# Kernel tuning notes

Measured on AMD Instinct MI355X. Metric: run time of the kernel, lower is better.

Reference implementation:

```python
import jax, jax.numpy as jnp
import numpy as np

EPS = 1e-6
TEMP_GEO = 0.07
W_LOCAL = 0.5
W_SHARP = 0.5


def _l2norm(x):
    return x / jnp.clip(jnp.linalg.norm(x, axis=-1, keepdims=True), 1e-12)


def setup_inputs() -> dict:
    key = jax.random.key(0)
    ks = jax.random.split(key, 6)
    B, L, S, C = 8, 1024, 1024, 128
    N, P = 8, 256
    q_geo = _l2norm(jax.random.normal(ks[0], (B, L, C), jnp.float32))
    geo_pos = _l2norm(jax.random.normal(ks[1], (B, S, C), jnp.float32))
    label = jax.random.randint(ks[2], (B, L, S), 0, 2, jnp.int32)
    q_cl = jax.random.normal(ks[3], (N, P, C), jnp.float32)
    cl_pos = jax.random.normal(ks[4], (N, P, C), jnp.float32)
    idx = jax.random.randint(ks[5], (N,), 0, P, jnp.int32)
    return {"q_geo": q_geo, "q_cl": q_cl, "geo_pos": geo_pos,
            "cl_pos": cl_pos, "label": label, "idx": idx}


def _masked_mean(v, m):
    # per-sample mean over the [L,S] plane of entries where m is True
    m = m.astype(v.dtype)
    return jnp.sum(v * m, axis=(1, 2)) / jnp.maximum(jnp.sum(m, axis=(1, 2)), 1.0)


def _loftr_loss(conf, label):
    # standard LoFTR coarse CE loss (LoFTRLoss source absent from repo snippet)
    conf = jnp.clip(conf, EPS, 1.0 - EPS)
    pos = label == 1
    neg = label == 0
    pos_loss = _masked_mean(-jnp.log(conf), pos)          # [B]
    neg_loss = _masked_mean(-jnp.log(1.0 - conf), neg)    # [B]
    loss = pos_loss + neg_loss
    return jnp.mean(loss), jnp.mean(pos_loss), jnp.mean(neg_loss)


def _geometric_loss(q, k, label):
    sim = jnp.einsum('blc,bsc->bls', q, k) / TEMP_GEO        # [B,L,S]
    conf = jax.nn.softmax(sim, axis=1) * jax.nn.softmax(sim, axis=2)
    return _loftr_loss(conf, label)


def _sharpness_loss(q, k, label):
    sim = (1.0 + jnp.einsum('blc,bsc->bls', q, k)) / 2.0     # [B,L,S]
    # column stats (over L, dim=0 per sample) -> sharpness1 [B,S]
    s1 = (jnp.max(sim, axis=1) - jnp.mean(sim, axis=1)) / jnp.std(sim, axis=1, ddof=1)
    sharp1 = jax.nn.softmax(s1, axis=-1)
    # row stats (over S, dim=1 per sample) -> sharpness2 [B,L]
    s2 = (jnp.max(sim, axis=2) - jnp.mean(sim, axis=2)) / jnp.std(sim, axis=2, ddof=1)
    sharp2 = jax.nn.softmax(s2, axis=-1)
    simc = jnp.clip(sim, EPS, 1.0 - EPS)
    nll = -jnp.log(simc)
    pos = (label == 1).astype(simc.dtype)
    neg = (label == 0)
    loss1 = jnp.sum(nll * sharp1[:, None, :] * pos, axis=(1, 2))   # [B]
    loss2 = jnp.sum(nll * sharp2[:, :, None] * pos, axis=(1, 2))   # [B]
    loss3 = _masked_mean(-jnp.log(1.0 - simc), neg)                # [B]
    losses = (loss1 + loss2) / 2.0 + loss3
    return sharp1, jnp.mean(losses)


def _contrast_loss(q, all_k):
    # intended math of GeCoContrast: full cosine matrix, diag positives, tail negatives
    N = q.shape[0]
    sim = (1.0 + _l2norm(q) @ _l2norm(all_k).T) / 2.0   # [N, M]
    sim = jnp.clip(sim, EPS, 1.0 - EPS)
    l_pos = jnp.diagonal(sim[:, :N])                    # [N]
    l_neg = sim[:, N:]                                  # [N, M-N]
    return (jnp.mean(-jnp.log(l_pos)) + jnp.mean(-jnp.log(1.0 - l_neg))) / 2.0


def _forward(q_geo, q_cl, geo_pos, cl_pos, label, idx):
    loss_geo, geo_pos_loss, geo_neg_loss = _geometric_loss(q_geo, geo_pos, label)
    sharpness, loss_sharp = _sharpness_loss(q_geo, geo_pos, label)
    loss_geo = ((1.0 - W_SHARP) * loss_geo + W_SHARP * loss_sharp) * W_LOCAL

    N, P, C = q_cl.shape
    ar = jnp.arange(N)
    q_sel = q_cl[ar, idx]                               # [N,C]
    sel = cl_pos[ar, idx]                               # [N,C] positives moved to slot 0
    first = cl_pos[:, 0, :]
    swapped = cl_pos.at[ar, idx].set(first).at[:, 0, :].set(sel)
    cl_pos_save = sel
    all_k = jnp.concatenate([swapped[:, 0, :],
                             swapped[:, 1:, :].reshape(N * (P - 1), C)], axis=0)
    loss_cl = _contrast_loss(q_sel, all_k) * (1.0 - W_LOCAL)

    total = loss_geo + loss_cl
    return (sharpness, cl_pos_save, total, geo_pos_loss, geo_neg_loss, loss_sharp, loss_cl)


def reference(q_geo, q_cl, geo_pos, cl_pos, label, idx):
    return _forward(q_geo, q_cl, geo_pos, cl_pos, label, idx)
```

## Files before the change

### kernel.cpp

```cpp
#include <hip/hip_runtime.h>
#include <math.h>

#define BB 8
#define LL 1024
#define SS 1024
#define CC 128
#define NN 8
#define PP 256

static constexpr float EPS       = 1e-6f;
static constexpr float ONE_M_EPS = 1.0f - 1e-6f;
static constexpr float INV_T     = 1.0f / 0.07f;
static constexpr float NLL_MAX   = 13.815511f;
static constexpr float NLL_MIN   = 1.0000005e-6f;

static constexpr size_t DOTSZ      = (size_t)BB * LL * SS;
static constexpr size_t OFF_LSER   = DOTSZ;
static constexpr size_t OFF_S2RAW  = DOTSZ + 8192;
static constexpr size_t OFF_LSEC   = DOTSZ + 16384;
static constexpr size_t OFF_S1RAW  = DOTSZ + 24576;
static constexpr size_t OFF_SHARP2 = DOTSZ + 32768;
static constexpr size_t OFF_RP     = DOTSZ + 40960;
static constexpr size_t OFF_CP     = OFF_RP + 524288;
static constexpr size_t OFF_ACC    = OFF_CP + 524288;
static constexpr size_t OFF_ACCCL  = OFF_ACC + 48;
static constexpr size_t OFF_QN     = OFF_ACC + 64;

static constexpr int OUT_CLSAVE = 8192;
static constexpr int OUT_SCAL   = 9216;

typedef __bf16 bf16x8 __attribute__((ext_vector_type(8)));
typedef float  floatx4 __attribute__((ext_vector_type(4)));

__device__ __forceinline__ bf16x8 mkfrag(unsigned a, unsigned b, unsigned c, unsigned d) {
    uint4 t = make_uint4(a, b, c, d);
    return __builtin_bit_cast(bf16x8, t);
}

__device__ __forceinline__ void split_f4(float4 x,
                                         unsigned& hp0, unsigned& hp1,
                                         unsigned& lp0, unsigned& lp1) {
    unsigned u0 = __builtin_bit_cast(unsigned, x.x);
    unsigned u1 = __builtin_bit_cast(unsigned, x.y);
    unsigned u2 = __builtin_bit_cast(unsigned, x.z);
    unsigned u3 = __builtin_bit_cast(unsigned, x.w);
    unsigned r0 = u0 + 0x7FFFu + ((u0 >> 16) & 1u);
    unsigned r1 = u1 + 0x7FFFu + ((u1 >> 16) & 1u);
    unsigned r2 = u2 + 0x7FFFu + ((u2 >> 16) & 1u);
    unsigned r3 = u3 + 0x7FFFu + ((u3 >> 16) & 1u);
    float s0 = x.x - __builtin_bit_cast(float, r0 & 0xFFFF0000u);
    float s1 = x.y - __builtin_bit_cast(float, r1 & 0xFFFF0000u);
    float s2 = x.z - __builtin_bit_cast(float, r2 & 0xFFFF0000u);
    float s3 = x.w - __builtin_bit_cast(float, r3 & 0xFFFF0000u);
    hp0 = __builtin_amdgcn_perm(r1, r0, 0x07060302u);
    hp1 = __builtin_amdgcn_perm(r3, r2, 0x07060302u);
    lp0 = __builtin_amdgcn_perm(__builtin_bit_cast(unsigned, s1),
                                __builtin_bit_cast(unsigned, s0), 0x07060302u);
    lp1 = __builtin_amdgcn_perm(__builtin_bit_cast(unsigned, s3),
                                __builtin_bit_cast(unsigned, s2), 0x07060302u);
}

__global__ __launch_bounds__(512) void prep(const float* __restrict__ q_cl,
                                            const float* __restrict__ cl_pos,
                                            const int* __restrict__ idx,
                                            float* __restrict__ out, float* __restrict__ ws) {
    int tid = threadIdx.x;
    if (tid < 50) ws[OFF_ACC + tid] = 0.0f;
    int n = tid >> 6, lane = tid & 63;
    int in = idx[n];
    const float* q = q_cl + ((size_t)(n * PP + in)) * CC;
    float2 qv = *(const float2*)(q + 2 * lane);
    float ss = qv.x * qv.x + qv.y * qv.y;
    for (int o = 32; o; o >>= 1) ss += __shfl_xor(ss, o);
    float inv = 1.0f / fmaxf(sqrtf(ss), 1e-12f);
    *(float2*)(ws + OFF_QN + n * 128 + 2 * lane) = make_float2(qv.x * inv, qv.y * inv);
    const float* cp = cl_pos + ((size_t)(n * PP + in)) * CC;
    float2 cv = *(const float2*)(cp + 2 * lane);
    *(float2*)(out + OUT_CLSAVE + n * 128 + 2 * lane) = cv;
}

__global__ __launch_bounds__(256) void gemm_dot(const float* __restrict__ A,
                                                const float* __restrict__ Bm,
                                                float* __restrict__ dot,
                                                float* __restrict__ ws) {
    int tid  = threadIdx.x;
    int lane = tid & 63;
    int w    = tid >> 6;
    int t    = blockIdx.x * 4 + w;
    int b    = t >> 8;
    int rem  = t & 255;
    int lt   = rem >> 4, st = rem & 15;
    int l0   = lt * 64, s0 = st * 64;
    int fl   = lane & 15;
    int quad = lane >> 4;

    const float* Ab = A  + ((size_t)b * LL + l0) * CC;
    const float* Bb = Bm + ((size_t)b * SS + s0) * CC;

    floatx4 acc[4][4];
#pragma unroll
    for (int i = 0; i < 4; i++)
#pragma unroll
        for (int j = 0; j < 4; j++) acc[i][j] = (floatx4){0.f, 0.f, 0.f, 0.f};

    for (int c0 = 0; c0 < 128; c0 += 32) {
        float4 ax[4][2], bx[4][2];
#pragma unroll
        for (int mt = 0; mt < 4; mt++) {
            const float* p = Ab + (size_t)(mt * 16 + fl) * CC + c0 + quad * 8;
            ax[mt][0] = *(const float4*)p;
            ax[mt][1] = *(const float4*)(p + 4);
        }
#pragma unroll
        for (int nt = 0; nt < 4; nt++) {
            const float* p = Bb + (size_t)(nt * 16 + fl) * CC + c0 + quad * 8;
            bx[nt][0] = *(const float4*)p;
            bx[nt][1] = *(const float4*)(p + 4);
        }
        bf16x8 ah[4], al[4];
#pragma unroll
        for (int mt = 0; mt < 4; mt++) {
            unsigned h0, h1, h2, h3, q0, q1, q2, q3;
            split_f4(ax[mt][0], h0, h1, q0, q1);
            split_f4(ax[mt][1], h2, h3, q2, q3);
            ah[mt] = mkfrag(h0, h1, h2, h3);
            al[mt] = mkfrag(q0, q1, q2, q3);
        }
#pragma unroll
        for (int nt = 0; nt < 4; nt++) {
            unsigned h0, h1, h2, h3, q0, q1, q2, q3;
            split_f4(bx[nt][0], h0, h1, q0, q1);
            split_f4(bx[nt][1], h2, h3, q2, q3);
            bf16x8 bh = mkfrag(h0, h1, h2, h3);
            bf16x8 bl = mkfrag(q0, q1, q2, q3);
#pragma unroll
            for (int mt = 0; mt < 4; mt++) {
                acc[mt][nt] = __builtin_amdgcn_mfma_f32_16x16x32_bf16(ah[mt], bh, acc[mt][nt], 0, 0, 0);
                acc[mt][nt] = __builtin_amdgcn_mfma_f32_16x16x32_bf16(ah[mt], bl, acc[mt][nt], 0, 0, 0);
                acc[mt][nt] = __builtin_amdgcn_mfma_f32_16x16x32_bf16(al[mt], bh, acc[mt][nt], 0, 0, 0);
            }
        }
    }

    float* D = dot + ((size_t)b * LL + l0) * SS + s0;
#pragma unroll
    for (int mt = 0; mt < 4; mt++)
#pragma unroll
        for (int nt = 0; nt < 4; nt++) {
            int col = nt * 16 + fl;
#pragma unroll
            for (int r = 0; r < 4; r++) {
                int row = mt * 16 + quad * 4 + r;
                D[(size_t)row * SS + col] = acc[mt][nt][r];
            }
        }

    float ces[4], cmx[4], csm[4], csq[4];
#pragma unroll
    for (int nt = 0; nt < 4; nt++) { ces[nt] = 0.f; cmx[nt] = -1e30f; csm[nt] = 0.f; csq[nt] = 0.f; }
#pragma unroll
    for (int mt = 0; mt < 4; mt++) {
#pragma unroll
        for (int r = 0; r < 4; r++) {
            float es = 0.f, mx = -1e30f, sm = 0.f, sq = 0.f;
#pragma unroll
            for (int nt = 0; nt < 4; nt++) {
                float d  = acc[mt][nt][r];
                float e  = __expf(d * INV_T);
                float s2 = fmaf(0.5f, d, 0.5f);
                es += e; mx = fmaxf(mx, s2); sm += s2; sq += s2 * s2;
                ces[nt] += e; cmx[nt] = fmaxf(cmx[nt], s2); csm[nt] += s2; csq[nt] += s2 * s2;
            }
            for (int o = 1; o < 16; o <<= 1) {
                es += __shfl_xor(es, o);
                mx = fmaxf(mx, __shfl_xor(mx, o));
                sm += __shfl_xor(sm, o);
                sq += __shfl_xor(sq, o);
            }
            if (fl == 0) {
                int row = l0 + mt * 16 + quad * 4 + r;
                *(float4*)(ws + OFF_RP + (((size_t)(b * 16 + st)) * 1024 + row) * 4) =
                    make_float4(es, mx, sm, sq);
            }
        }
    }
#pragma unroll
    for (int nt = 0; nt < 4; nt++) {
        float es = ces[nt], mx = cmx[nt], sm = csm[nt], sq = csq[nt];
        for (int o = 16; o < 64; o <<= 1) {
            es += __shfl_xor(es, o);
            mx = fmaxf(mx, __shfl_xor(mx, o));
            sm += __shfl_xor(sm, o);
            sq += __shfl_xor(sq, o);
        }
        if (quad == 0) {
            int col = s0 + nt * 16 + fl;
            *(float4*)(ws + OFF_CP + (((size_t)(b * 16 + lt)) * 1024 + col) * 4) =
                make_float4(es, mx, sm, sq);
        }
    }
}

__global__ __launch_bounds__(256) void rc_combine(float* __restrict__ ws) {
    int g = (blockIdx.x & 31) * 256 + threadIdx.x;
    bool docol = blockIdx.x >= 32;
    int b = g >> 10, i = g & 1023;
    const float* part = ws + (docol ? OFF_CP : OFF_RP);
    float es = 0.f, mx = -1e30f, sm = 0.f, sq = 0.f;
#pragma unroll
    for (int t = 0; t < 16; t++) {
        float4 v = *(const float4*)(part + (((size_t)(b * 16 + t)) * 1024 + i) * 4);
        es += v.x; mx = fmaxf(mx, v.y); sm += v.z; sq += v.w;
    }
    float mean = sm * (1.0f / 1024.0f);
    float var  = (sq - sm * sm * (1.0f / 1024.0f)) * (1.0f / 1023.0f);
    float zs   = (mx - mean) / sqrtf(fmaxf(var, 1e-30f));
    if (!docol) {
        ws[OFF_LSER + g]  = __logf(es);
        ws[OFF_S2RAW + g] = zs;
    } else {
        ws[OFF_LSEC + g]  = __logf(es);
        ws[OFF_S1RAW + g] = zs;
    }
}

__global__ __launch_bounds__(256) void softmax16(float* __restrict__ ws, float* __restrict__ out) {
    int q = blockIdx.x;
    int b = q & 7;
    const float* src = ws + ((q < 8) ? OFF_S1RAW : OFF_S2RAW) + (size_t)b * 1024;
    float* dst = (q < 8) ? (out + (size_t)b * 1024) : (ws + OFF_SHARP2 + (size_t)b * 1024);
    float4 v = ((const float4*)src)[threadIdx.x];
    int lane = threadIdx.x & 63, wid = threadIdx.x >> 6;
    __shared__ float sb[4];
    __shared__ float red;
    float mx = fmaxf(fmaxf(v.x, v.y), fmaxf(v.z, v.w));
    for (int o = 32; o; o >>= 1) mx = fmaxf(mx, __shfl_xor(mx, o));
    if (!lane) sb[wid] = mx;
    __syncthreads();
    if (threadIdx.x == 0) red = fmaxf(fmaxf(sb[0], sb[1]), fmaxf(sb[2], sb[3]));
    __syncthreads();
    mx = red;
    float e0 = __expf(v.x - mx), e1 = __expf(v.y - mx), e2 = __expf(v.z - mx), e3 = __expf(v.w - mx);
    float sm = e0 + e1 + e2 + e3;
    for (int o = 32; o; o >>= 1) sm += __shfl_xor(sm, o);
    __syncthreads();
    if (!lane) sb[wid] = sm;
    __syncthreads();
    if (threadIdx.x == 0) red = sb[0] + sb[1] + sb[2] + sb[3];
    __syncthreads();
    float inv = 1.0f / red;
    ((float4*)dst)[threadIdx.x] = make_float4(e0 * inv, e1 * inv, e2 * inv, e3 * inv);
}

__device__ __forceinline__ void proc_elem(float d, int lab, float lcj, float sh1j,
                                          float lr, float s2v,
                                          float& posg, float& negg, float& l1, float& l2,
                                          float& negs, float& pcf) {
    float t = lr + lcj - d * (2.0f * INV_T);
    float isPos = (lab == 1) ? 1.0f : 0.0f;
    float isNeg = 1.0f - isPos;
    float tp   = fminf(fmaxf(t, NLL_MIN), NLL_MAX);
    float simc = fminf(fmaxf(fmaf(0.5f, d, 0.5f), EPS), ONE_M_EPS);
    float om   = fminf(fmaxf(fmaf(-0.5f, d, 0.5f), EPS), ONE_M_EPS);
    float nll2 = -__logf(simc);
    float cf   = fminf(fmaxf(__expf(-t), EPS), ONE_M_EPS);
    float nllg = -__logf(1.0f - cf);
    float nlls = -__logf(om);
    posg += isPos * tp;
    l1   += isPos * nll2 * sh1j;
    l2   += isPos * nll2 * s2v;
    pcf  += isPos;
    negg += isNeg * nllg;
    negs += isNeg * nlls;
}

__global__ __launch_bounds__(256) void main_loss(const float* __restrict__ dot,
                                                 const int* __restrict__ label,
                                                 const float* __restrict__ sharp1,
                                                 float* __restrict__ ws) {
    int b = blockIdx.y;
    int l0 = blockIdx.x * 4;
    int s = threadIdx.x * 4;
    float4 lc4 = *(const float4*)(ws + OFF_LSEC + (size_t)b * 1024 + s);
    float4 sh1 = *(const float4*)(sharp1 + (size_t)b * 1024 + s);
    const float* lser = ws + OFF_LSER + (size_t)b * 1024;
    const float* sh2  = ws + OFF_SHARP2 + (size_t)b * 1024;
    float posg = 0, negg = 0, l1 = 0, l2 = 0, negs = 0, pcf = 0;
#pragma unroll
    for (int r = 0; r < 4; r++) {
        int l = l0 + r;
        float lr  = lser[l];
        float s2v = sh2[l];
        size_t base = ((size_t)(b * 1024 + l)) * 1024 + s;
        float4 d4 = *(const float4*)(dot + base);
        int4  lb  = *(const int4*)(label + base);
        proc_elem(d4.x, lb.x, lc4.x, sh1.x, lr, s2v, posg, negg, l1, l2, negs, pcf);
        proc_elem(d4.y, lb.y, lc4.y, sh1.y, lr, s2v, posg, negg, l1, l2, negs, pcf);
        proc_elem(d4.z, lb.z, lc4.z, sh1.z, lr, s2v, posg, negg, l1, l2, negs, pcf);
        proc_elem(d4.w, lb.w, lc4.w, sh1.w, lr, s2v, posg, negg, l1, l2, negs, pcf);
    }
    float vals[6] = {posg, negg, l1, l2, negs, pcf};
    __shared__ float sb[6][4];
    int lane = threadIdx.x & 63, wid = threadIdx.x >> 6;
#pragma unroll
    for (int k = 0; k < 6; k++) {
        float v = vals[k];
        for (int o = 32; o; o >>= 1) v += __shfl_xor(v, o);
        if (!lane) sb[k][wid] = v;
    }
    __syncthreads();
    if (threadIdx.x < 6) {
        float r = sb[threadIdx.x][0] + sb[threadIdx.x][1] + sb[threadIdx.x][2] + sb[threadIdx.x][3];
        atomicAdd(ws + OFF_ACC + (size_t)b * 6 + threadIdx.x, r);
    }
}

__global__ __launch_bounds__(256) void contrast(const float* __restrict__ cl_pos,
                                                const int* __restrict__ idx,
                                                float* __restrict__ ws) {
    int j = blockIdx.x * 4 + (threadIdx.x >> 6);
    int lane = threadIdx.x & 63;
    int m, p;
    if (j < NN) {
        m = j; p = idx[j];
    } else {
        int jj = j - NN;
        m = jj / (PP - 1);
        p = 1 + (jj - m * (PP - 1));
        if (p == idx[m]) p = 0;
    }
    const float* k = cl_pos + ((size_t)(m * PP + p)) * CC;
    float2 kv = *(const float2*)(k + 2 * lane);
    float ksq = kv.x * kv.x + kv.y * kv.y;
    for (int o = 32; o; o >>= 1) ksq += __shfl_xor(ksq, o);
    float invkn = 1.0f / fmaxf(sqrtf(ksq), 1e-12f);
    float pos = 0.0f, neg = 0.0f;
    if (j < NN) {
        const float2 qv = *(const float2*)(ws + OFF_QN + j * 128 + 2 * lane);
        float dt = qv.x * kv.x + qv.y * kv.y;
        for (int o = 32; o; o >>= 1) dt += __shfl_xor(dt, o);
        float sim = fminf(fmaxf(fmaf(0.5f * invkn, dt, 0.5f), EPS), ONE_M_EPS);
        pos = -__logf(sim);
    } else {
#pragma unroll
        for (int n = 0; n < NN; n++) {
            const float2 qv = *(const float2*)(ws + OFF_QN + n * 128 + 2 * lane);
            float dt = qv.x * kv.x + qv.y * kv.y;
            for (int o = 32; o; o >>= 1) dt += __shfl_xor(dt, o);
            float om = fminf(fmaxf(fmaf(-0.5f * invkn, dt, 0.5f), EPS), ONE_M_EPS);
            neg -= __logf(om);
        }
    }
    __shared__ float sb[2][4];
    int w = threadIdx.x >> 6;
    if (!lane) { sb[0][w] = pos; sb[1][w] = neg; }
    __syncthreads();
    if (threadIdx.x == 0) {
        float ps = sb[0][0] + sb[0][1] + sb[0][2] + sb[0][3];
        float ng = sb[1][0] + sb[1][1] + sb[1][2] + sb[1][3];
        if (ps != 0.0f) atomicAdd(ws + OFF_ACCCL + 0, ps);
        if (ng != 0.0f) atomicAdd(ws + OFF_ACCCL + 1, ng);
    }
}

__global__ void finalize(float* __restrict__ out, const float* __restrict__ ws) {
    if (threadIdx.x != 0) return;
    float gp = 0, gn = 0, lsh = 0;
    for (int b = 0; b < 8; b++) {
        const float* a = ws + OFF_ACC + (size_t)b * 6;
        float pc = a[5];
        float nc = (float)((size_t)LL * SS) - pc;
        gp += a[0] / fmaxf(pc, 1.0f);
        gn += a[1] / fmaxf(nc, 1.0f);
        lsh += (a[2] + a[3]) * 0.5f + a[4] / fmaxf(nc, 1.0f);
    }
    gp *= 0.125f; gn *= 0.125f; lsh *= 0.125f;
    float lgeo = gp + gn;
    float lgw = (0.5f * lgeo + 0.5f * lsh) * 0.5f;
    float clp = ws[OFF_ACCCL + 0] / 8.0f;
    float cln = ws[OFF_ACCCL + 1] / (8.0f * 2040.0f);
    float lcl = (clp + cln) * 0.5f * 0.5f;
    out[OUT_SCAL + 0] = lgw + lcl;
    out[OUT_SCAL + 1] = gp;
    out[OUT_SCAL + 2] = gn;
    out[OUT_SCAL + 3] = lsh;
    out[OUT_SCAL + 4] = lcl;
}

extern "C" void kernel_launch(void* const* d_in, const int* in_sizes, int n_in,
                              void* d_out, int out_size, void* d_ws, size_t ws_size,
                              hipStream_t stream) {
    const float* q_geo   = (const float*)d_in[0];
    const float* q_cl    = (const float*)d_in[1];
    const float* geo_pos = (const float*)d_in[2];
    const float* cl_pos  = (const float*)d_in[3];
    const int*   label   = (const int*)d_in[4];
    const int*   idx     = (const int*)d_in[5];
    float* out = (float*)d_out;
    float* ws  = (float*)d_ws;
    float* dot = ws;

    prep<<<dim3(1), dim3(512), 0, stream>>>(q_cl, cl_pos, idx, out, ws);
    gemm_dot<<<dim3(512), dim3(256), 0, stream>>>(q_geo, geo_pos, dot, ws);
    rc_combine<<<dim3(64), dim3(256), 0, stream>>>(ws);
    softmax16<<<dim3(16), dim3(256), 0, stream>>>(ws, out);
    main_loss<<<dim3(256, 8), dim3(256), 0, stream>>>(dot, label, out, ws);
    contrast<<<dim3(512), dim3(256), 0, stream>>>(cl_pos, idx, ws);
    finalize<<<dim3(1), dim3(64), 0, stream>>>(out, ws);
}
```

Baseline: 163.7 us.

## Merge seven kernel launches into three with fused contrast, combine and finalize

Folds the prep and contrastive-loss work into extra blocks of the GEMM kernel, so they run alongside the GEMM tiles. Merges the row/column partial combine with the sharpness softmax into one kernel. Finalizes the scalar losses from the last main-loss block through an atomic completion counter instead of a separate launch. This removes launch overhead and serialization of small kernels, at the cost of a counter reset in the first kernel and extra synchronization logic.

```diff
diff --git a/kernel.cpp b/kernel.cpp
--- a/kernel.cpp
+++ b/kernel.cpp
@@ -16,15 +16,13 @@
 
 static constexpr size_t DOTSZ      = (size_t)BB * LL * SS;
 static constexpr size_t OFF_LSER   = DOTSZ;
-static constexpr size_t OFF_S2RAW  = DOTSZ + 8192;
 static constexpr size_t OFF_LSEC   = DOTSZ + 16384;
-static constexpr size_t OFF_S1RAW  = DOTSZ + 24576;
 static constexpr size_t OFF_SHARP2 = DOTSZ + 32768;
 static constexpr size_t OFF_RP     = DOTSZ + 40960;
 static constexpr size_t OFF_CP     = OFF_RP + 524288;
 static constexpr size_t OFF_ACC    = OFF_CP + 524288;
-static constexpr size_t OFF_ACCCL  = OFF_ACC + 48;
-static constexpr size_t OFF_QN     = OFF_ACC + 64;
+static constexpr size_t OFF_DONE   = OFF_ACC + 48;
+static constexpr size_t OFF_CLP    = OFF_ACC + 64;
 
 static constexpr int OUT_CLSAVE = 8192;
 static constexpr int OUT_SCAL   = 9216;
@@ -60,196 +58,241 @@
                                 __builtin_bit_cast(unsigned, s2), 0x07060302u);
 }
 
-__global__ __launch_bounds__(512) void prep(const float* __restrict__ q_cl,
-                                            const float* __restrict__ cl_pos,
-                                            const int* __restrict__ idx,
-                                            float* __restrict__ out, float* __restrict__ ws) {
-    int tid = threadIdx.x;
-    if (tid < 50) ws[OFF_ACC + tid] = 0.0f;
-    int n = tid >> 6, lane = tid & 63;
-    int in = idx[n];
-    const float* q = q_cl + ((size_t)(n * PP + in)) * CC;
-    float2 qv = *(const float2*)(q + 2 * lane);
-    float ss = qv.x * qv.x + qv.y * qv.y;
-    for (int o = 32; o; o >>= 1) ss += __shfl_xor(ss, o);
-    float inv = 1.0f / fmaxf(sqrtf(ss), 1e-12f);
-    *(float2*)(ws + OFF_QN + n * 128 + 2 * lane) = make_float2(qv.x * inv, qv.y * inv);
-    const float* cp = cl_pos + ((size_t)(n * PP + in)) * CC;
-    float2 cv = *(const float2*)(cp + 2 * lane);
-    *(float2*)(out + OUT_CLSAVE + n * 128 + 2 * lane) = cv;
-}
-
-__global__ __launch_bounds__(256) void gemm_dot(const float* __restrict__ A,
-                                                const float* __restrict__ Bm,
-                                                float* __restrict__ dot,
-                                                float* __restrict__ ws) {
+__global__ __launch_bounds__(256) void k1_gemm(const float* __restrict__ A,
+                                               const float* __restrict__ Bm,
+                                               const float* __restrict__ q_cl,
+                                               const float* __restrict__ cl_pos,
+                                               const int* __restrict__ idx,
+                                               float* __restrict__ dot,
+                                               float* __restrict__ ws,
+                                               float* __restrict__ out) {
+    __shared__ float qn[8][128];
+    __shared__ float sbc[2][4];
     int tid  = threadIdx.x;
     int lane = tid & 63;
     int w    = tid >> 6;
-    int t    = blockIdx.x * 4 + w;
-    int b    = t >> 8;
-    int rem  = t & 255;
-    int lt   = rem >> 4, st = rem & 15;
-    int l0   = lt * 64, s0 = st * 64;
-    int fl   = lane & 15;
-    int quad = lane >> 4;
-
-    const float* Ab = A  + ((size_t)b * LL + l0) * CC;
-    const float* Bb = Bm + ((size_t)b * SS + s0) * CC;
-
-    floatx4 acc[4][4];
-#pragma unroll
-    for (int i = 0; i < 4; i++)
-#pragma unroll
-        for (int j = 0; j < 4; j++) acc[i][j] = (floatx4){0.f, 0.f, 0.f, 0.f};
-
-    for (int c0 = 0; c0 < 128; c0 += 32) {
-        float4 ax[4][2], bx[4][2];
+
+    if (blockIdx.x < 512) {
+        int t    = blockIdx.x * 4 + w;
+        int b    = t >> 8;
+        int rem  = t & 255;
+        int lt   = rem >> 4, st = rem & 15;
+        int l0   = lt * 64, s0 = st * 64;
+        int fl   = lane & 15;
+        int quad = lane >> 4;
+
+        const float* Ab = A  + ((size_t)b * LL + l0) * CC;
+        const float* Bb = Bm + ((size_t)b * SS + s0) * CC;
+
+        floatx4 acc[4][4];
+#pragma unroll
+        for (int i = 0; i < 4; i++)
+#pragma unroll
+            for (int j = 0; j < 4; j++) acc[i][j] = (floatx4){0.f, 0.f, 0.f, 0.f};
+
+        for (int c0 = 0; c0 < 128; c0 += 32) {
+            float4 ax[4][2], bx[4][2];
+#pragma unroll
+            for (int mt = 0; mt < 4; mt++) {
+                const float* p = Ab + (size_t)(mt * 16 + fl) * CC + c0 + quad * 8;
+                ax[mt][0] = *(const float4*)p;
+                ax[mt][1] = *(const float4*)(p + 4);
+            }
+#pragma unroll
+            for (int nt = 0; nt < 4; nt++) {
+                const float* p = Bb + (size_t)(nt * 16 + fl) * CC + c0 + quad * 8;
+                bx[nt][0] = *(const float4*)p;
+                bx[nt][1] = *(const float4*)(p + 4);
+            }
+            bf16x8 ah[4], al[4];
+#pragma unroll
+            for (int mt = 0; mt < 4; mt++) {
+                unsigned h0, h1, h2, h3, q0, q1, q2, q3;
+                split_f4(ax[mt][0], h0, h1, q0, q1);
+                split_f4(ax[mt][1], h2, h3, q2, q3);
+                ah[mt] = mkfrag(h0, h1, h2, h3);
+                al[mt] = mkfrag(q0, q1, q2, q3);
+            }
+#pragma unroll
+            for (int nt = 0; nt < 4; nt++) {
+                unsigned h0, h1, h2, h3, q0, q1, q2, q3;
+                split_f4(bx[nt][0], h0, h1, q0, q1);
+                split_f4(bx[nt][1], h2, h3, q2, q3);
+                bf16x8 bh = mkfrag(h0, h1, h2, h3);
+                bf16x8 bl = mkfrag(q0, q1, q2, q3);
+#pragma unroll
+                for (int mt = 0; mt < 4; mt++) {
+                    acc[mt][nt] = __builtin_amdgcn_mfma_f32_16x16x32_bf16(ah[mt], bh, acc[mt][nt], 0, 0, 0);
+                    acc[mt][nt] = __builtin_amdgcn_mfma_f32_16x16x32_bf16(ah[mt], bl, acc[mt][nt], 0, 0, 0);
+                    acc[mt][nt] = __builtin_amdgcn_mfma_f32_16x16x32_bf16(al[mt], bh, acc[mt][nt], 0, 0, 0);
+                }
+            }
+        }
+
+        float* D = dot + ((size_t)b * LL + l0) * SS + s0;
+#pragma unroll
+        for (int mt = 0; mt < 4; mt++)
+#pragma unroll
+            for (int nt = 0; nt < 4; nt++) {
+                int col = nt * 16 + fl;
+#pragma unroll
+                for (int r = 0; r < 4; r++) {
+                    int row = mt * 16 + quad * 4 + r;
+                    D[(size_t)row * SS + col] = acc[mt][nt][r];
+                }
+            }
+
+        float ces[4], cmx[4], csm[4], csq[4];
+#pragma unroll
+        for (int nt = 0; nt < 4; nt++) { ces[nt] = 0.f; cmx[nt] = -1e30f; csm[nt] = 0.f; csq[nt] = 0.f; }
 #pragma unroll
         for (int mt = 0; mt < 4; mt++) {
-            const float* p = Ab + (size_t)(mt * 16 + fl) * CC + c0 + quad * 8;
-            ax[mt][0] = *(const float4*)p;
-            ax[mt][1] = *(const float4*)(p + 4);
+#pragma unroll
+            for (int r = 0; r < 4; r++) {
+                float es = 0.f, mx = -1e30f, sm = 0.f, sq = 0.f;
+#pragma unroll
+                for (int nt = 0; nt < 4; nt++) {
+                    float d  = acc[mt][nt][r];
+                    float e  = __expf(d * INV_T);
+                    float s2 = fmaf(0.5f, d, 0.5f);
+                    es += e; mx = fmaxf(mx, s2); sm += s2; sq += s2 * s2;
+                    ces[nt] += e; cmx[nt] = fmaxf(cmx[nt], s2); csm[nt] += s2; csq[nt] += s2 * s2;
+                }
+                for (int o = 1; o < 16; o <<= 1) {
+                    es += __shfl_xor(es, o);
+                    mx = fmaxf(mx, __shfl_xor(mx, o));
+                    sm += __shfl_xor(sm, o);
+                    sq += __shfl_xor(sq, o);
+                }
+                if (fl == 0) {
+                    int row = l0 + mt * 16 + quad * 4 + r;
+                    *(float4*)(ws + OFF_RP + (((size_t)(b * 16 + st)) * 1024 + row) * 4) =
+                        make_float4(es, mx, sm, sq);
+                }
+            }
         }
 #pragma unroll
         for (int nt = 0; nt < 4; nt++) {
-            const float* p = Bb + (size_t)(nt * 16 + fl) * CC + c0 + quad * 8;
-            bx[nt][0] = *(const float4*)p;
-            bx[nt][1] = *(const float4*)(p + 4);
-        }
-        bf16x8 ah[4], al[4];
-#pragma unroll
-        for (int mt = 0; mt < 4; mt++) {
-            unsigned h0, h1, h2, h3, q0, q1, q2, q3;
-            split_f4(ax[mt][0], h0, h1, q0, q1);
-            split_f4(ax[mt][1], h2, h3, q2, q3);
-            ah[mt] = mkfrag(h0, h1, h2, h3);
-            al[mt] = mkfrag(q0, q1, q2, q3);
-        }
-#pragma unroll
-        for (int nt = 0; nt < 4; nt++) {
-            unsigned h0, h1, h2, h3, q0, q1, q2, q3;
-            split_f4(bx[nt][0], h0, h1, q0, q1);
-            split_f4(bx[nt][1], h2, h3, q2, q3);
-            bf16x8 bh = mkfrag(h0, h1, h2, h3);
-            bf16x8 bl = mkfrag(q0, q1, q2, q3);
-#pragma unroll
-            for (int mt = 0; mt < 4; mt++) {
-                acc[mt][nt] = __builtin_amdgcn_mfma_f32_16x16x32_bf16(ah[mt], bh, acc[mt][nt], 0, 0, 0);
-                acc[mt][nt] = __builtin_amdgcn_mfma_f32_16x16x32_bf16(ah[mt], bl, acc[mt][nt], 0, 0, 0);
-                acc[mt][nt] = __builtin_amdgcn_mfma_f32_16x16x32_bf16(al[mt], bh, acc[mt][nt], 0, 0, 0);
-            }
-        }
-    }
-
-    float* D = dot + ((size_t)b * LL + l0) * SS + s0;
-#pragma unroll
-    for (int mt = 0; mt < 4; mt++)
-#pragma unroll
-        for (int nt = 0; nt < 4; nt++) {
-            int col = nt * 16 + fl;
-#pragma unroll
-            for (int r = 0; r < 4; r++) {
-                int row = mt * 16 + quad * 4 + r;
-                D[(size_t)row * SS + col] = acc[mt][nt][r];
-            }
-        }
-
-    float ces[4], cmx[4], csm[4], csq[4];
-#pragma unroll
-    for (int nt = 0; nt < 4; nt++) { ces[nt] = 0.f; cmx[nt] = -1e30f; csm[nt] = 0.f; csq[nt] = 0.f; }
-#pragma unroll
-    for (int mt = 0; mt < 4; mt++) {
-#pragma unroll
-        for (int r = 0; r < 4; r++) {
-            float es = 0.f, mx = -1e30f, sm = 0.f, sq = 0.f;
-#pragma unroll
-            for (int nt = 0; nt < 4; nt++) {
-                float d  = acc[mt][nt][r];
-                float e  = __expf(d * INV_T);
-                float s2 = fmaf(0.5f, d, 0.5f);
-                es += e; mx = fmaxf(mx, s2); sm += s2; sq += s2 * s2;
-                ces[nt] += e; cmx[nt] = fmaxf(cmx[nt], s2); csm[nt] += s2; csq[nt] += s2 * s2;
-            }
-            for (int o = 1; o < 16; o <<= 1) {
+            float es = ces[nt], mx = cmx[nt], sm = csm[nt], sq = csq[nt];
+            for (int o = 16; o < 64; o <<= 1) {
                 es += __shfl_xor(es, o);
                 mx = fmaxf(mx, __shfl_xor(mx, o));
                 sm += __shfl_xor(sm, o);
                 sq += __shfl_xor(sq, o);
             }
-            if (fl == 0) {
-                int row = l0 + mt * 16 + quad * 4 + r;
-                *(float4*)(ws + OFF_RP + (((size_t)(b * 16 + st)) * 1024 + row) * 4) =
+            if (quad == 0) {
+                int col = s0 + nt * 16 + fl;
+                *(float4*)(ws + OFF_CP + (((size_t)(b * 16 + lt)) * 1024 + col) * 4) =
                     make_float4(es, mx, sm, sq);
             }
         }
-    }
-#pragma unroll
-    for (int nt = 0; nt < 4; nt++) {
-        float es = ces[nt], mx = cmx[nt], sm = csm[nt], sq = csq[nt];
-        for (int o = 16; o < 64; o <<= 1) {
-            es += __shfl_xor(es, o);
-            mx = fmaxf(mx, __shfl_xor(mx, o));
-            sm += __shfl_xor(sm, o);
-            sq += __shfl_xor(sq, o);
-        }
-        if (quad == 0) {
-            int col = s0 + nt * 16 + fl;
-            *(float4*)(ws + OFF_CP + (((size_t)(b * 16 + lt)) * 1024 + col) * 4) =
-                make_float4(es, mx, sm, sq);
-        }
-    }
-}
-
-__global__ __launch_bounds__(256) void rc_combine(float* __restrict__ ws) {
-    int g = (blockIdx.x & 31) * 256 + threadIdx.x;
-    bool docol = blockIdx.x >= 32;
-    int b = g >> 10, i = g & 1023;
-    const float* part = ws + (docol ? OFF_CP : OFF_RP);
-    float es = 0.f, mx = -1e30f, sm = 0.f, sq = 0.f;
-#pragma unroll
-    for (int t = 0; t < 16; t++) {
-        float4 v = *(const float4*)(part + (((size_t)(b * 16 + t)) * 1024 + i) * 4);
-        es += v.x; mx = fmaxf(mx, v.y); sm += v.z; sq += v.w;
-    }
-    float mean = sm * (1.0f / 1024.0f);
-    float var  = (sq - sm * sm * (1.0f / 1024.0f)) * (1.0f / 1023.0f);
-    float zs   = (mx - mean) / sqrtf(fmaxf(var, 1e-30f));
-    if (!docol) {
-        ws[OFF_LSER + g]  = __logf(es);
-        ws[OFF_S2RAW + g] = zs;
+    } else if (blockIdx.x < 544) {
+        int cb = blockIdx.x - 512;
+#pragma unroll
+        for (int i = 0; i < 2; i++) {
+            int n = 2 * w + i;
+            int in = idx[n];
+            float2 qv = *(const float2*)(q_cl + ((size_t)(n * PP + in)) * CC + 2 * lane);
+            float ss = qv.x * qv.x + qv.y * qv.y;
+            for (int o = 32; o; o >>= 1) ss += __shfl_xor(ss, o);
+            float inv = 1.0f / fmaxf(sqrtf(ss), 1e-12f);
+            qn[n][2 * lane]     = qv.x * inv;
+            qn[n][2 * lane + 1] = qv.y * inv;
+        }
+        __syncthreads();
+        float pos = 0.f, neg = 0.f;
+        for (int jj = 0; jj < 16; jj++) {
+            int j = cb * 64 + w * 16 + jj;
+            int m, p;
+            if (j < NN) { m = j; p = idx[j]; }
+            else {
+                int t2 = j - NN;
+                m = t2 / (PP - 1);
+                p = 1 + (t2 - m * (PP - 1));
+                if (p == idx[m]) p = 0;
+            }
+            const float* k = cl_pos + ((size_t)(m * PP + p)) * CC;
+            float2 kv = *(const float2*)(k + 2 * lane);
+            float ksq = kv.x * kv.x + kv.y * kv.y;
+            for (int o = 32; o; o >>= 1) ksq += __shfl_xor(ksq, o);
+            float invkn = 1.0f / fmaxf(sqrtf(ksq), 1e-12f);
+            if (j < NN) {
+                float dt = qn[j][2 * lane] * kv.x + qn[j][2 * lane + 1] * kv.y;
+                for (int o = 32; o; o >>= 1) dt += __shfl_xor(dt, o);
+                float sim = fminf(fmaxf(fmaf(0.5f * invkn, dt, 0.5f), EPS), ONE_M_EPS);
+                pos += -__logf(sim);
+            } else {
+#pragma unroll
+                for (int n = 0; n < NN; n++) {
+                    float dt = qn[n][2 * lane] * kv.x + qn[n][2 * lane + 1] * kv.y;
+                    for (int o = 32; o; o >>= 1) dt += __shfl_xor(dt, o);
+                    float om = fminf(fmaxf(fmaf(-0.5f * invkn, dt, 0.5f), EPS), ONE_M_EPS);
+                    neg -= __logf(om);
+                }
+            }
+        }
+        if (!lane) { sbc[0][w] = pos; sbc[1][w] = neg; }
+        __syncthreads();
+        if (tid == 0) {
+            ws[OFF_CLP + cb * 2 + 0] = sbc[0][0] + sbc[0][1] + sbc[0][2] + sbc[0][3];
+            ws[OFF_CLP + cb * 2 + 1] = sbc[1][0] + sbc[1][1] + sbc[1][2] + sbc[1][3];
+        }
     } else {
-        ws[OFF_LSEC + g]  = __logf(es);
-        ws[OFF_S1RAW + g] = zs;
-    }
-}
-
-__global__ __launch_bounds__(256) void softmax16(float* __restrict__ ws, float* __restrict__ out) {
+        if (tid < 48) ws[OFF_ACC + tid] = 0.0f;
+        if (tid == 48) *(unsigned*)(ws + OFF_DONE) = 0u;
+        int n = tid >> 5, c = (tid & 31) * 4;
+        int in = idx[n];
+        float4 v = *(const float4*)(cl_pos + ((size_t)(n * PP + in)) * CC + c);
+        *(float4*)(out + OUT_CLSAVE + n * 128 + c) = v;
+    }
+}
+
+__global__ __launch_bounds__(256) void k2_comb(float* __restrict__ ws, float* __restrict__ out) {
     int q = blockIdx.x;
     int b = q & 7;
-    const float* src = ws + ((q < 8) ? OFF_S1RAW : OFF_S2RAW) + (size_t)b * 1024;
-    float* dst = (q < 8) ? (out + (size_t)b * 1024) : (ws + OFF_SHARP2 + (size_t)b * 1024);
-    float4 v = ((const float4*)src)[threadIdx.x];
-    int lane = threadIdx.x & 63, wid = threadIdx.x >> 6;
+    bool docol = q >= 8;
+    int tid = threadIdx.x;
+    const float* part = ws + (docol ? OFF_CP : OFF_RP);
+    int i0 = tid * 4;
+    float zs[4], lse[4];
+#pragma unroll
+    for (int k = 0; k < 4; k++) {
+        int i = i0 + k;
+        float es = 0.f, mx = -1e30f, sm = 0.f, sq = 0.f;
+#pragma unroll
+        for (int t = 0; t < 16; t++) {
+            float4 v = *(const float4*)(part + (((size_t)(b * 16 + t)) * 1024 + i) * 4);
+            es += v.x; mx = fmaxf(mx, v.y); sm += v.z; sq += v.w;
+        }
+        lse[k] = __logf(es);
+        float mean = sm * (1.0f / 1024.0f);
+        float var  = (sq - sm * sm * (1.0f / 1024.0f)) * (1.0f / 1023.0f);
+        zs[k] = (mx - mean) / sqrtf(fmaxf(var, 1e-30f));
+    }
+    *(float4*)(ws + (docol ? OFF_LSEC : OFF_LSER) + (size_t)b * 1024 + i0) =
+        make_float4(lse[0], lse[1], lse[2], lse[3]);
+
+    int lane = tid & 63, wid = tid >> 6;
     __shared__ float sb[4];
     __shared__ float red;
-    float mx = fmaxf(fmaxf(v.x, v.y), fmaxf(v.z, v.w));
+    float mx = fmaxf(fmaxf(zs[0], zs[1]), fmaxf(zs[2], zs[3]));
     for (int o = 32; o; o >>= 1) mx = fmaxf(mx, __shfl_xor(mx, o));
     if (!lane) sb[wid] = mx;
     __syncthreads();
-    if (threadIdx.x == 0) red = fmaxf(fmaxf(sb[0], sb[1]), fmaxf(sb[2], sb[3]));
+    if (tid == 0) red = fmaxf(fmaxf(sb[0], sb[1]), fmaxf(sb[2], sb[3]));
     __syncthreads();
     mx = red;
-    float e0 = __expf(v.x - mx), e1 = __expf(v.y - mx), e2 = __expf(v.z - mx), e3 = __expf(v.w - mx);
+    float e0 = __expf(zs[0] - mx), e1 = __expf(zs[1] - mx), e2 = __expf(zs[2] - mx), e3 = __expf(zs[3] - mx);
     float sm = e0 + e1 + e2 + e3;
     for (int o = 32; o; o >>= 1) sm += __shfl_xor(sm, o);
     __syncthreads();
     if (!lane) sb[wid] = sm;
     __syncthreads();
-    if (threadIdx.x == 0) red = sb[0] + sb[1] + sb[2] + sb[3];
+    if (tid == 0) red = sb[0] + sb[1] + sb[2] + sb[3];
     __syncthreads();
     float inv = 1.0f / red;
-    ((float4*)dst)[threadIdx.x] = make_float4(e0 * inv, e1 * inv, e2 * inv, e3 * inv);
+    float* dst = docol ? (out + (size_t)b * 1024) : (ws + OFF_SHARP2 + (size_t)b * 1024);
+    *(float4*)(dst + i0) = make_float4(e0 * inv, e1 * inv, e2 * inv, e3 * inv);
 }
 
 __device__ __forceinline__ void proc_elem(float d, int lab, float lcj, float sh1j,
@@ -274,10 +317,11 @@
     negs += isNeg * nlls;
 }
 
-__global__ __launch_bounds__(256) void main_loss(const float* __restrict__ dot,
-                                                 const int* __restrict__ label,
-                                                 const float* __restrict__ sharp1,
-                                                 float* __restrict__ ws) {
+__global__ __launch_bounds__(256) void k3_loss(const float* __restrict__ dot,
+                                               const int* __restrict__ label,
+                                               const float* __restrict__ sharp1,
+                                               float* __restrict__ ws,
+                                               float* __restrict__ out) {
     int b = blockIdx.y;
     int l0 = blockIdx.x * 4;
     int s = threadIdx.x * 4;
@@ -313,78 +357,43 @@
         float r = sb[threadIdx.x][0] + sb[threadIdx.x][1] + sb[threadIdx.x][2] + sb[threadIdx.x][3];
         atomicAdd(ws + OFF_ACC + (size_t)b * 6 + threadIdx.x, r);
     }
-}
-
-__global__ __launch_bounds__(256) void contrast(const float* __restrict__ cl_pos,
-                                                const int* __restrict__ idx,
-                                                float* __restrict__ ws) {
-    int j = blockIdx.x * 4 + (threadIdx.x >> 6);
-    int lane = threadIdx.x & 63;
-    int m, p;
-    if (j < NN) {
-        m = j; p = idx[j];
-    } else {
-        int jj = j - NN;
-        m = jj / (PP - 1);
-        p = 1 + (jj - m * (PP - 1));
-        if (p == idx[m]) p = 0;
-    }
-    const float* k = cl_pos + ((size_t)(m * PP + p)) * CC;
-    float2 kv = *(const float2*)(k + 2 * lane);
-    float ksq = kv.x * kv.x + kv.y * kv.y;
-    for (int o = 32; o; o >>= 1) ksq += __shfl_xor(ksq, o);
-    float invkn = 1.0f / fmaxf(sqrtf(ksq), 1e-12f);
-    float pos = 0.0f, neg = 0.0f;
-    if (j < NN) {
-        const float2 qv = *(const float2*)(ws + OFF_QN + j * 128 + 2 * lane);
-        float dt = qv.x * kv.x + qv.y * kv.y;
-        for (int o = 32; o; o >>= 1) dt += __shfl_xor(dt, o);
-        float sim = fminf(fmaxf(fmaf(0.5f * invkn, dt, 0.5f), EPS), ONE_M_EPS);
-        pos = -__logf(sim);
-    } else {
-#pragma unroll
-        for (int n = 0; n < NN; n++) {
-            const float2 qv = *(const float2*)(ws + OFF_QN + n * 128 + 2 * lane);
-            float dt = qv.x * kv.x + qv.y * kv.y;
-            for (int o = 32; o; o >>= 1) dt += __shfl_xor(dt, o);
-            float om = fminf(fmaxf(fmaf(-0.5f * invkn, dt, 0.5f), EPS), ONE_M_EPS);
-            neg -= __logf(om);
-        }
-    }
-    __shared__ float sb[2][4];
-    int w = threadIdx.x >> 6;
-    if (!lane) { sb[0][w] = pos; sb[1][w] = neg; }
     __syncthreads();
     if (threadIdx.x == 0) {
-        float ps = sb[0][0] + sb[0][1] + sb[0][2] + sb[0][3];
-        float ng = sb[1][0] + sb[1][1] + sb[1][2] + sb[1][3];
-        if (ps != 0.0f) atomicAdd(ws + OFF_ACCCL + 0, ps);
-        if (ng != 0.0f) atomicAdd(ws + OFF_ACCCL + 1, ng);
-    }
-}
-
-__global__ void finalize(float* __restrict__ out, const float* __restrict__ ws) {
-    if (threadIdx.x != 0) return;
-    float gp = 0, gn = 0, lsh = 0;
-    for (int b = 0; b < 8; b++) {
-        const float* a = ws + OFF_ACC + (size_t)b * 6;
-        float pc = a[5];
-        float nc = (float)((size_t)LL * SS) - pc;
-        gp += a[0] / fmaxf(pc, 1.0f);
-        gn += a[1] / fmaxf(nc, 1.0f);
-        lsh += (a[2] + a[3]) * 0.5f + a[4] / fmaxf(nc, 1.0f);
-    }
-    gp *= 0.125f; gn *= 0.125f; lsh *= 0.125f;
-    float lgeo = gp + gn;
-    float lgw = (0.5f * lgeo + 0.5f * lsh) * 0.5f;
-    float clp = ws[OFF_ACCCL + 0] / 8.0f;
-    float cln = ws[OFF_ACCCL + 1] / (8.0f * 2040.0f);
-    float lcl = (clp + cln) * 0.5f * 0.5f;
-    out[OUT_SCAL + 0] = lgw + lcl;
-    out[OUT_SCAL + 1] = gp;
-    out[OUT_SCAL + 2] = gn;
-    out[OUT_SCAL + 3] = lsh;
-    out[OUT_SCAL + 4] = lcl;
+        __threadfence();
+        unsigned prev = __hip_atomic_fetch_add((unsigned*)(ws + OFF_DONE), 1u,
+                                               __ATOMIC_ACQ_REL, __HIP_MEMORY_SCOPE_AGENT);
+        if (prev == 2048u - 1u) {
+            float gp = 0, gn = 0, lsh = 0;
+            for (int b2 = 0; b2 < 8; b2++) {
+                float a[6];
+#pragma unroll
+                for (int k = 0; k < 6; k++)
+                    a[k] = __hip_atomic_load(ws + OFF_ACC + b2 * 6 + k,
+                                             __ATOMIC_RELAXED, __HIP_MEMORY_SCOPE_AGENT);
+                float pc = a[5];
+                float nc = (float)((size_t)LL * SS) - pc;
+                gp += a[0] / fmaxf(pc, 1.0f);
+                gn += a[1] / fmaxf(nc, 1.0f);
+                lsh += (a[2] + a[3]) * 0.5f + a[4] / fmaxf(nc, 1.0f);
+            }
+            gp *= 0.125f; gn *= 0.125f; lsh *= 0.125f;
+            float lgeo = gp + gn;
+            float lgw = (0.5f * lgeo + 0.5f * lsh) * 0.5f;
+            float clp = 0.f, cln = 0.f;
+            for (int c = 0; c < 32; c++) {
+                clp += ws[OFF_CLP + 2 * c + 0];
+                cln += ws[OFF_CLP + 2 * c + 1];
+            }
+            clp /= 8.0f;
+            cln /= (8.0f * 2040.0f);
+            float lcl = (clp + cln) * 0.5f * 0.5f;
+            out[OUT_SCAL + 0] = lgw + lcl;
+            out[OUT_SCAL + 1] = gp;
+            out[OUT_SCAL + 2] = gn;
+            out[OUT_SCAL + 3] = lsh;
+            out[OUT_SCAL + 4] = lcl;
+        }
+    }
 }
 
 extern "C" void kernel_launch(void* const* d_in, const int* in_sizes, int n_in,
@@ -400,11 +409,7 @@
     float* ws  = (float*)d_ws;
     float* dot = ws;
 
-    prep<<<dim3(1), dim3(512), 0, stream>>>(q_cl, cl_pos, idx, out, ws);
-    gemm_dot<<<dim3(512), dim3(256), 0, stream>>>(q_geo, geo_pos, dot, ws);
-    rc_combine<<<dim3(64), dim3(256), 0, stream>>>(ws);
-    softmax16<<<dim3(16), dim3(256), 0, stream>>>(ws, out);
-    main_loss<<<dim3(256, 8), dim3(256), 0, stream>>>(dot, label, out, ws);
-    contrast<<<dim3(512), dim3(256), 0, stream>>>(cl_pos, idx, ws);
-    finalize<<<dim3(1), dim3(64), 0, stream>>>(out, ws);
-}
+    k1_gemm<<<dim3(545), dim3(256), 0, stream>>>(q_geo, geo_pos, q_cl, cl_pos, idx, dot, ws, out);
+    k2_comb<<<dim3(16), dim3(256), 0, stream>>>(ws, out);
+    k3_loss<<<dim3(256, 8), dim3(256), 0, stream>>>(dot, label, out, ws, out);
+}
```

Measured after the change: 256.9 us. 56.9% more time.
